# Kernel optimization log

Measured on AMD Instinct MI355X. Metric: run time of the kernel, lower is better.

The kernel has to match this reference:

```python
import jax, jax.numpy as jnp
import numpy as np

N_NODES = 200000
N_EDGES = 240000
HIDDEN = 128
N_TYPES = 6


def setup_inputs() -> dict:
    key = jax.random.key(0)
    k1, k2, k3, k4, k5 = jax.random.split(key, 5)
    state_embedding = jax.random.normal(k1, (N_NODES, HIDDEN), dtype=jnp.float32)
    # row 0: edge type in [1, N_TYPES]; row 1: source node; row 2: target node
    etype = jax.random.randint(k2, (N_EDGES,), 1, N_TYPES + 1, dtype=jnp.int32)
    src = jax.random.randint(k3, (N_EDGES,), 0, N_NODES, dtype=jnp.int32)
    tgt = jax.random.randint(k4, (N_EDGES,), 0, N_NODES, dtype=jnp.int32)
    typed_edges = jnp.stack([etype, src, tgt], axis=0)  # [3, E]
    # stacked per-edge-type Linear(2H, H, bias=False) weights, applied as x @ W[t]
    W = jax.random.normal(k5, (N_TYPES, 2 * HIDDEN, HIDDEN), dtype=jnp.float32) / np.sqrt(2 * HIDDEN)
    return {"state_embedding": state_embedding, "typed_edges": typed_edges, "W": W}


def reference(state_embedding, typed_edges, W):
    etype, src, tgt = typed_edges[0], typed_edges[1], typed_edges[2]
    # gather source/target node states and concat -> [E, 2H]
    x = jnp.concatenate([state_embedding[src], state_embedding[tgt]], axis=1)
    n_types = W.shape[0]
    msgs = jnp.zeros((x.shape[0], W.shape[2]), dtype=x.dtype)
    # fixed small loop over edge types; masking replaces the dynamic boolean
    # filtering of the torch code (edges with type t use only W[t-1])
    for t in range(n_types):
        mask = (etype == t + 1)[:, None]
        msgs = msgs + jnp.where(mask, x @ W[t], jnp.zeros((), x.dtype))
    # scatter-add messages into target node slots, dim_size = num nodes
    return jax.ops.segment_sum(msgs, tgt, num_segments=state_embedding.shape[0])
```

## Files before the change

### kernel.cpp

```cpp
#include <hip/hip_runtime.h>

#define NTYPES 6
#define HID 128
#define E_TILE 64
#define TPB 4
#define TNBITS 19
#define TNMASK ((1 << TNBITS) - 1)

typedef short short8 __attribute__((ext_vector_type(8)));
typedef float f32x4 __attribute__((ext_vector_type(4)));

static __device__ __forceinline__ ushort f2bf(float f) {
    union { float f; unsigned u; } v; v.f = f;
    unsigned r = v.u + 0x7FFFu + ((v.u >> 16) & 1u);
    return (ushort)(r >> 16);
}


__global__ void k_prep(int4* __restrict__ zp, int n4,
                       const float* __restrict__ Sf, ushort* __restrict__ Sb, int total,
                       const float* __restrict__ W, ushort* __restrict__ Wt,
                       int zb, int sb) {
    int b = blockIdx.x;
    if (b < zb) {
        int i = b * 256 + threadIdx.x;
        if (i < n4) zp[i] = make_int4(0, 0, 0, 0);
    } else if (b < zb + sb) {
        int g = ((b - zb) * 256 + threadIdx.x) * 8;
        if (g < total) {
            float4 a = *(const float4*)(Sf + g);
            float4 c = *(const float4*)(Sf + g + 4);
            ushort t[8] = { f2bf(a.x), f2bf(a.y), f2bf(a.z), f2bf(a.w),
                            f2bf(c.x), f2bf(c.y), f2bf(c.z), f2bf(c.w) };
            *(short8*)(Sb + g) = *(short8*)t;
        }
    } else {
        int t = (b - zb - sb) * 256 + threadIdx.x;
        int n  = t & 127;
        int k8 = (t >> 7) & 31;
        int ty = t >> 12;
        if (ty >= NTYPES) return;
        const float* wp = W + ((size_t)ty * 256 + (size_t)k8 * 8) * HID + n;
        ushort tmp[8];
        #pragma unroll
        for (int j = 0; j < 8; ++j) tmp[j] = f2bf(wp[(size_t)j * HID]);
        *(short8*)(Wt + ((size_t)ty * HID + n) * 256 + k8 * 8) = *(short8*)tmp;
    }
}

template <int RANK>
__global__ void k_bin(const int* __restrict__ etype, const int* __restrict__ src,
                      const int* __restrict__ tgt, int E, int CAP,
                      int* __restrict__ hdr, int* __restrict__ ncnt,
                      int2* __restrict__ sortedT2) {
    __shared__ int lcnt[NTYPES];
    __shared__ int lbase[NTYPES];
    if (threadIdx.x < NTYPES) lcnt[threadIdx.x] = 0;
    __syncthreads();
    int i = blockIdx.x * 256 + threadIdx.x;
    bool valid = (i < E);
    int sn = 0, pk = 0, t = 0, lrk = 0;
    if (valid) {
        t  = etype[i] - 1;
        int tn = tgt[i];
        sn = src[i];
        int a = 0;
        if (RANK) a = atomicAdd(&ncnt[tn], 1);
        pk  = tn | (a << TNBITS);
        lrk = atomicAdd(&lcnt[t], 1);
    }
    __syncthreads();
    if (threadIdx.x < NTYPES) {
        int c = lcnt[threadIdx.x];
        lbase[threadIdx.x] = c ? atomicAdd(&hdr[16 + threadIdx.x], c) : 0;
    }
    __syncthreads();
    if (valid) {
        int pos = lbase[t] + lrk;
        if (pos < CAP) sortedT2[(size_t)t * CAP + pos] = make_int2(sn, pk);
    }
}

__global__ void k_scan1(const int* __restrict__ ncnt, int* __restrict__ noff,
                        int* __restrict__ bsum, int N) {
    __shared__ int s[256];
    const int b = blockIdx.x, t = threadIdx.x;
    const int base = b * 1024 + t * 4;
    int v[4];
    #pragma unroll
    for (int i = 0; i < 4; ++i) v[i] = (base + i < N) ? ncnt[base + i] : 0;
    int tsum = v[0] + v[1] + v[2] + v[3];
    s[t] = tsum;
    __syncthreads();
    for (int off = 1; off < 256; off <<= 1) {
        int x = (t >= off) ? s[t - off] : 0;
        __syncthreads();
        s[t] += x;
        __syncthreads();
    }
    if (t == 255) bsum[b] = s[255];
    int run = s[t] - tsum;
    #pragma unroll
    for (int i = 0; i < 4; ++i)
        if (base + i < N) { noff[base + i] = run; run += v[i]; }
}

__global__ void k_scan2(int* __restrict__ bsum, int nb) {
    __shared__ int s[256];
    const int t = threadIdx.x;
    int v = (t < nb) ? bsum[t] : 0;
    s[t] = v;
    __syncthreads();
    for (int off = 1; off < 256; off <<= 1) {
        int x = (t >= off) ? s[t - off] : 0;
        __syncthreads();
        s[t] += x;
        __syncthreads();
    }
    if (t < nb) bsum[t] = s[t] - v;
}

template <int MODE>
__launch_bounds__(256, 4)
__global__ void k_gemm(const ushort* __restrict__ Sb, const float* __restrict__ Sf,
                       const ushort* __restrict__ Wt, const int* __restrict__ hdr,
                       const int2* __restrict__ sortedT2, int CAP,
                       const int* __restrict__ ncnt, const int* __restrict__ noff,
                       const int* __restrict__ bsum,
                       ushort* __restrict__ msgs, float* __restrict__ out) {
    __shared__ __align__(16) ushort Xs[E_TILE][264];
    __shared__ int sN[TPB][E_TILE];
    __shared__ int tN[TPB][E_TILE];
    __shared__ int dstR[TPB][E_TILE];

    int g = blockIdx.x;
    int ty, t0 = 0, ntl = 0, cnt_t = 0;
    for (ty = 0; ty < NTYPES; ++ty) {
        int c = hdr[16 + ty];
        if (c > CAP) c = CAP;
        int nt = (c + E_TILE - 1) >> 6;
        int ng = (nt + TPB - 1) / TPB;
        if (g < ng) {
            t0 = g * TPB;
            ntl = nt - t0; if (ntl > TPB) ntl = TPB;
            cnt_t = c;
            break;
        }
        g -= ng;
    }
    if (ty == NTYPES) return;

    const int tid = threadIdx.x;
    const int w  = tid >> 6;
    const int l  = tid & 63;
    const int lr = l & 15;
    const int lg = l >> 4;

    {
        const int tt = tid >> 6, s = l;
        if (tt < ntl) {
            int gp = (t0 + tt) * E_TILE + s;
            int sn = 0, tn = 0, dr = 0;
            if (gp < cnt_t) {
                int2 v = sortedT2[(size_t)ty * CAP + gp];
                sn = v.x;
                tn = v.y & TNMASK;
                if (MODE == 2) {
                    int a = ((unsigned)v.y) >> TNBITS;
                    dr = (ncnt[tn] == 1) ? -(tn + 1)
                                         : (noff[tn] + bsum[tn >> 10] + a);
                }
            }
            sN[tt][s] = sn; tN[tt][s] = tn; dstR[tt][s] = dr;
        }
    }
    __syncthreads();

    const ushort* wb = Wt + ((size_t)ty * HID + w * 32 + lr) * 256 + 8 * lg;

    for (int tt = 0; tt < ntl; ++tt) {
        int cnt = cnt_t - (t0 + tt) * E_TILE;
        if (cnt > E_TILE) cnt = E_TILE;

        {
            const int e = tid >> 2, q = tid & 3;
            ushort* dp = &Xs[e][q * 64];
            if (e < cnt) {
                const int node = (q & 2) ? tN[tt][e] : sN[tt][e];
                if (MODE == 2) {
                    const ushort* rp = Sb + (size_t)node * HID + (q & 1) * 64;
                    short8 v[8];
                    #pragma unroll
                    for (int i = 0; i < 8; ++i) v[i] = *(const short8*)(rp + i * 8);
                    #pragma unroll
                    for (int i = 0; i < 8; ++i) *(short8*)(dp + i * 8) = v[i];
                } else {
                    const float* rp = Sf + (size_t)node * HID + (q & 1) * 64;
                    #pragma unroll
                    for (int i = 0; i < 8; ++i) {
                        float4 a = *(const float4*)(rp + i * 8);
                        float4 b = *(const float4*)(rp + i * 8 + 4);
                        ushort tmp[8] = { f2bf(a.x), f2bf(a.y), f2bf(a.z), f2bf(a.w),
                                          f2bf(b.x), f2bf(b.y), f2bf(b.z), f2bf(b.w) };
                        *(short8*)(dp + i * 8) = *(short8*)tmp;
                    }
                }
            } else {
                short8 z = (short8){0, 0, 0, 0, 0, 0, 0, 0};
                #pragma unroll
                for (int i = 0; i < 8; ++i) *(short8*)(dp + i * 8) = z;
            }
        }
        __syncthreads();

        f32x4 acc[4][2];
        #pragma unroll
        for (int mf = 0; mf < 4; ++mf)
            #pragma unroll
            for (int nf = 0; nf < 2; ++nf)
                acc[mf][nf] = (f32x4){0.f, 0.f, 0.f, 0.f};

        const ushort* xb = &Xs[lr][8 * lg];
        #pragma unroll
        for (int kk = 0; kk < 8; ++kk) {
            const int k0 = kk * 32;
            short8 b0 = *(const short8*)(wb + k0);
            short8 b1 = *(const short8*)(wb + 16 * 256 + k0);
            #pragma unroll
            for (int mf = 0; mf < 4; ++mf) {
                short8 a = *(const short8*)(xb + mf * 16 * 264 + k0);
                acc[mf][0] = __builtin_amdgcn_mfma_f32_16x16x32_bf16(a, b0, acc[mf][0], 0, 0, 0);
                acc[mf][1] = __builtin_amdgcn_mfma_f32_16x16x32_bf16(a, b1, acc[mf][1], 0, 0, 0);
            }
        }
        __syncthreads();

        float (*Os)[132] = (float (*)[132])&Xs[0][0];
        #pragma unroll
        for (int mf = 0; mf < 4; ++mf)
            #pragma unroll
            for (int nf = 0; nf < 2; ++nf)
                #pragma unroll
                for (int r = 0; r < 4; ++r)
                    Os[mf * 16 + lg * 4 + r][w * 32 + nf * 16 + lr] = acc[mf][nf][r];
        __syncthreads();

        if (MODE == 2) {
            const int r8e = tid >> 4, cg = tid & 15;
            #pragma unroll
            for (int rr = 0; rr < 4; ++rr) {
                int row = rr * 16 + r8e;
                if (row < cnt) {
                    int dr = dstR[tt][row];
                    float4 a = *(const float4*)&Os[row][cg * 8];
                    float4 b = *(const float4*)&Os[row][cg * 8 + 4];
                    if (dr >= 0) {
                        ushort tmp[8] = { f2bf(a.x), f2bf(a.y), f2bf(a.z), f2bf(a.w),
                                          f2bf(b.x), f2bf(b.y), f2bf(b.z), f2bf(b.w) };
                        *(short8*)(msgs + (size_t)dr * HID + cg * 8) = *(short8*)tmp;
                    } else {
                        float* op = out + (size_t)(-dr - 1) * HID + cg * 8;
                        *(float4*)op = a;
                        *(float4*)(op + 4) = b;
                    }
                }
            }
        } else {
            const int rA = tid >> 7;
            const int c  = tid & (HID - 1);
            for (int it = 0; it < E_TILE / 2; ++it) {
                int ee = it * 2 + rA;
                if (ee < cnt) atomicAdd(&out[(size_t)tN[tt][ee] * HID + c], Os[ee][c]);
            }
        }
        __syncthreads();
    }
}

__launch_bounds__(256)
__global__ void k_scatter(const ushort* __restrict__ msgs, const int* __restrict__ noff,
                          const int* __restrict__ bsum, float* __restrict__ out,
                          int N, int Etot) {
    int node = blockIdx.x * 4 + (threadIdx.x >> 6);
    if (node >= N) return;
    int cp = threadIdx.x & 63;
    int s = noff[node] + bsum[node >> 10];
    int e = (node + 1 < N) ? (noff[node + 1] + bsum[(node + 1) >> 10]) : Etot;
    if (e - s == 1) return;
    float a0 = 0.f, a1 = 0.f;
    for (int r = s; r < e; ++r) {
        unsigned u = *(const unsigned*)(msgs + (size_t)r * HID + cp * 2);
        union { unsigned u; float f; } lo, hi;
        lo.u = u << 16; hi.u = u & 0xFFFF0000u;
        a0 += lo.f; a1 += hi.f;
    }
    *(float2*)(out + (size_t)node * HID + cp * 2) = make_float2(a0, a1);
}

extern "C" void kernel_launch(void* const* d_in, const int* in_sizes, int n_in,
                              void* d_out, int out_size, void* d_ws, size_t ws_size,
                              hipStream_t stream) {
    const float* Sf    = (const float*)d_in[0];
    const int*   edges = (const int*)d_in[1];
    const float* W     = (const float*)d_in[2];
    float* out = (float*)d_out;

    const int E = in_sizes[1] / 3;
    const int N = in_sizes[0] / HID;
    const int* etype = edges;
    const int* src   = edges + E;
    const int* tgt   = edges + 2 * E;
    int* ws = (int*)d_ws;

    const int CAP = E / 5 + 4096;

    int* ncnt = ws + 32;
    int* noff = ncnt + N;
    int* bsum = noff + N + 1;
    size_t intsEnd = (size_t)(32 + N + (N + 1) + 256) * sizeof(int);
    size_t st2Off  = (intsEnd + 255) & ~(size_t)255;
    size_t wtOff   = ((st2Off + (size_t)NTYPES * CAP * sizeof(int2)) + 255) & ~(size_t)255;
    size_t sbOff   = ((wtOff + (size_t)NTYPES * HID * 256 * 2) + 255) & ~(size_t)255;
    size_t msgsOff = ((sbOff + (size_t)N * HID * 2) + 255) & ~(size_t)255;
    size_t need2   = msgsOff + (size_t)E * HID * 2;

    const int nb1 = (N + 1023) / 1024;
    const int eb  = (E + 255) / 256;
    const int nblocks = (E + E_TILE * TPB - 1) / (E_TILE * TPB) + 2 * NTYPES;
    ushort* Wt = (ushort*)((char*)d_ws + wtOff);
    int2* sortedT2 = (int2*)((char*)d_ws + st2Off);

    if (ws_size >= need2 && nb1 <= 256 && N < (1 << TNBITS)) {
        ushort* Sb   = (ushort*)((char*)d_ws + sbOff);
        ushort* msgs = (ushort*)((char*)d_ws + msgsOff);
        const int total = N * HID;
        const int n4 = (32 + N + 3) / 4;
        const int zb = (n4 + 255) / 256;
        const int sb = (total / 8 + 255) / 256;
        const int wb = (NTYPES * HID * 32 + 255) / 256;

        k_prep<<<zb + sb + wb, 256, 0, stream>>>((int4*)ws, n4, Sf, Sb, total, W, Wt, zb, sb);
        k_bin<1><<<eb, 256, 0, stream>>>(etype, src, tgt, E, CAP, ws, ncnt, sortedT2);
        k_scan1<<<nb1, 256, 0, stream>>>(ncnt, noff, bsum, N);
        k_scan2<<<1, 256, 0, stream>>>(bsum, nb1);
        k_gemm<2><<<nblocks, 256, 0, stream>>>(Sb, Sf, Wt, ws, sortedT2, CAP,
                                               ncnt, noff, bsum, msgs, out);
        k_scatter<<<(N + 3) / 4, 256, 0, stream>>>(msgs, noff, bsum, out, N, E);
    } else {
        int2* sortedT0 = (int2*)((char*)d_ws + 256);
        ushort* Wt0 = (ushort*)((char*)d_ws + 256 +
                      (((size_t)NTYPES * CAP * sizeof(int2) + 255) & ~(size_t)255));

        k_prep<<<1 + (NTYPES * HID * 32 + 255) / 256, 256, 0, stream>>>(
            (int4*)ws, 8, nullptr, nullptr, 0, W, Wt0, 1, 0);
        hipMemsetAsync(d_out, 0, (size_t)out_size * sizeof(float), stream);
        k_bin<0><<<eb, 256, 0, stream>>>(etype, src, tgt, E, CAP, ws, nullptr, sortedT0);
        k_gemm<0><<<nblocks, 256, 0, stream>>>(nullptr, Sf, Wt0, ws, sortedT0, CAP,
                                               nullptr, nullptr, nullptr, nullptr, out);
    }
}
```

Baseline: 132.0 us.

## Prefetch next edge tile into registers and pack degree-1 flag into offsets

The bf16 gather of the next tile's source and target node rows is now issued into registers before the current tile's MFMA work, so global-load latency can overlap compute. A degree-1 flag is packed into the high bit of each node offset during the scan, so the gemm and scatter kernels skip reading the separate count array and the next node's offset for degree-1 nodes. The prefetch raises register pressure under a launch bound of four blocks per CU, and the packed flag limits offsets to 30 bits.

```diff
diff --git a/kernel.cpp b/kernel.cpp
--- a/kernel.cpp
+++ b/kernel.cpp
@@ -6,6 +6,8 @@
 #define TPB 4
 #define TNBITS 19
 #define TNMASK ((1 << TNBITS) - 1)
+#define DEG1F 0x40000000
+#define OFFM  0x3FFFFFFF
 
 typedef short short8 __attribute__((ext_vector_type(8)));
 typedef float f32x4 __attribute__((ext_vector_type(4)));
@@ -102,7 +104,10 @@
     int run = s[t] - tsum;
     #pragma unroll
     for (int i = 0; i < 4; ++i)
-        if (base + i < N) { noff[base + i] = run; run += v[i]; }
+        if (base + i < N) {
+            noff[base + i] = run | ((v[i] == 1) ? DEG1F : 0);
+            run += v[i];
+        }
 }
 
 __global__ void k_scan2(int* __restrict__ bsum, int nb) {
@@ -125,8 +130,7 @@
 __global__ void k_gemm(const ushort* __restrict__ Sb, const float* __restrict__ Sf,
                        const ushort* __restrict__ Wt, const int* __restrict__ hdr,
                        const int2* __restrict__ sortedT2, int CAP,
-                       const int* __restrict__ ncnt, const int* __restrict__ noff,
-                       const int* __restrict__ bsum,
+                       const int* __restrict__ noff, const int* __restrict__ bsum,
                        ushort* __restrict__ msgs, float* __restrict__ out) {
     __shared__ __align__(16) ushort Xs[E_TILE][264];
     __shared__ int sN[TPB][E_TILE];
@@ -167,8 +171,9 @@
                 tn = v.y & TNMASK;
                 if (MODE == 2) {
                     int a = ((unsigned)v.y) >> TNBITS;
-                    dr = (ncnt[tn] == 1) ? -(tn + 1)
-                                         : (noff[tn] + bsum[tn >> 10] + a);
+                    int nf_ = noff[tn];
+                    dr = (nf_ & DEG1F) ? -(tn + 1)
+                                       : ((nf_ & OFFM) + bsum[tn >> 10] + a);
                 }
             }
             sN[tt][s] = sn; tN[tt][s] = tn; dstR[tt][s] = dr;
@@ -177,41 +182,64 @@
     __syncthreads();
 
     const ushort* wb = Wt + ((size_t)ty * HID + w * 32 + lr) * 256 + 8 * lg;
+
+    const int e_ = tid >> 2, q_ = tid & 3;
+    const short8 z8 = (short8){0, 0, 0, 0, 0, 0, 0, 0};
+    short8 pv[8];
+
+    if (MODE == 2) {
+        int cnt0 = cnt_t - t0 * E_TILE; if (cnt0 > E_TILE) cnt0 = E_TILE;
+        if (e_ < cnt0) {
+            const int node = (q_ & 2) ? tN[0][e_] : sN[0][e_];
+            const ushort* rp = Sb + (size_t)node * HID + (q_ & 1) * 64;
+            #pragma unroll
+            for (int i = 0; i < 8; ++i) pv[i] = *(const short8*)(rp + i * 8);
+        } else {
+            #pragma unroll
+            for (int i = 0; i < 8; ++i) pv[i] = z8;
+        }
+    }
 
     for (int tt = 0; tt < ntl; ++tt) {
         int cnt = cnt_t - (t0 + tt) * E_TILE;
         if (cnt > E_TILE) cnt = E_TILE;
 
-        {
-            const int e = tid >> 2, q = tid & 3;
-            ushort* dp = &Xs[e][q * 64];
-            if (e < cnt) {
-                const int node = (q & 2) ? tN[tt][e] : sN[tt][e];
-                if (MODE == 2) {
-                    const ushort* rp = Sb + (size_t)node * HID + (q & 1) * 64;
-                    short8 v[8];
-                    #pragma unroll
-                    for (int i = 0; i < 8; ++i) v[i] = *(const short8*)(rp + i * 8);
-                    #pragma unroll
-                    for (int i = 0; i < 8; ++i) *(short8*)(dp + i * 8) = v[i];
-                } else {
-                    const float* rp = Sf + (size_t)node * HID + (q & 1) * 64;
-                    #pragma unroll
-                    for (int i = 0; i < 8; ++i) {
-                        float4 a = *(const float4*)(rp + i * 8);
-                        float4 b = *(const float4*)(rp + i * 8 + 4);
-                        ushort tmp[8] = { f2bf(a.x), f2bf(a.y), f2bf(a.z), f2bf(a.w),
-                                          f2bf(b.x), f2bf(b.y), f2bf(b.z), f2bf(b.w) };
-                        *(short8*)(dp + i * 8) = *(short8*)tmp;
-                    }
+        if (MODE == 2) {
+            ushort* dp = &Xs[e_][q_ * 64];
+            #pragma unroll
+            for (int i = 0; i < 8; ++i) *(short8*)(dp + i * 8) = pv[i];
+        } else {
+            ushort* dp = &Xs[e_][q_ * 64];
+            if (e_ < cnt) {
+                const int node = (q_ & 2) ? tN[tt][e_] : sN[tt][e_];
+                const float* rp = Sf + (size_t)node * HID + (q_ & 1) * 64;
+                #pragma unroll
+                for (int i = 0; i < 8; ++i) {
+                    float4 a = *(const float4*)(rp + i * 8);
+                    float4 b = *(const float4*)(rp + i * 8 + 4);
+                    ushort tmp[8] = { f2bf(a.x), f2bf(a.y), f2bf(a.z), f2bf(a.w),
+                                      f2bf(b.x), f2bf(b.y), f2bf(b.z), f2bf(b.w) };
+                    *(short8*)(dp + i * 8) = *(short8*)tmp;
                 }
             } else {
-                short8 z = (short8){0, 0, 0, 0, 0, 0, 0, 0};
-                #pragma unroll
-                for (int i = 0; i < 8; ++i) *(short8*)(dp + i * 8) = z;
-            }
-        }
-        __syncthreads();
+                #pragma unroll
+                for (int i = 0; i < 8; ++i) *(short8*)(dp + i * 8) = z8;
+            }
+        }
+        __syncthreads();
+
+        if (MODE == 2 && tt + 1 < ntl) {
+            int cntn = cnt_t - (t0 + tt + 1) * E_TILE; if (cntn > E_TILE) cntn = E_TILE;
+            if (e_ < cntn) {
+                const int node = (q_ & 2) ? tN[tt + 1][e_] : sN[tt + 1][e_];
+                const ushort* rp = Sb + (size_t)node * HID + (q_ & 1) * 64;
+                #pragma unroll
+                for (int i = 0; i < 8; ++i) pv[i] = *(const short8*)(rp + i * 8);
+            } else {
+                #pragma unroll
+                for (int i = 0; i < 8; ++i) pv[i] = z8;
+            }
+        }
 
         f32x4 acc[4][2];
         #pragma unroll
@@ -283,10 +311,11 @@
                           int N, int Etot) {
     int node = blockIdx.x * 4 + (threadIdx.x >> 6);
     if (node >= N) return;
+    int raw = noff[node];
+    if (raw & DEG1F) return;
     int cp = threadIdx.x & 63;
-    int s = noff[node] + bsum[node >> 10];
-    int e = (node + 1 < N) ? (noff[node + 1] + bsum[(node + 1) >> 10]) : Etot;
-    if (e - s == 1) return;
+    int s = (raw & OFFM) + bsum[node >> 10];
+    int e = (node + 1 < N) ? ((noff[node + 1] & OFFM) + bsum[(node + 1) >> 10]) : Etot;
     float a0 = 0.f, a1 = 0.f;
     for (int r = s; r < e; ++r) {
         unsigned u = *(const unsigned*)(msgs + (size_t)r * HID + cp * 2);
@@ -344,7 +373,7 @@
         k_scan1<<<nb1, 256, 0, stream>>>(ncnt, noff, bsum, N);
         k_scan2<<<1, 256, 0, stream>>>(bsum, nb1);
         k_gemm<2><<<nblocks, 256, 0, stream>>>(Sb, Sf, Wt, ws, sortedT2, CAP,
-                                               ncnt, noff, bsum, msgs, out);
+                                               noff, bsum, msgs, out);
         k_scatter<<<(N + 3) / 4, 256, 0, stream>>>(msgs, noff, bsum, out, N, E);
     } else {
         int2* sortedT0 = (int2*)((char*)d_ws + 256);
@@ -356,6 +385,6 @@
         hipMemsetAsync(d_out, 0, (size_t)out_size * sizeof(float), stream);
         k_bin<0><<<eb, 256, 0, stream>>>(etype, src, tgt, E, CAP, ws, nullptr, sortedT0);
         k_gemm<0><<<nblocks, 256, 0, stream>>>(nullptr, Sf, Wt0, ws, sortedT0, CAP,
-                                               nullptr, nullptr, nullptr, nullptr, out);
-    }
-}
+                                               nullptr, nullptr, nullptr, out);
+    }
+}
```

Measured after the change: 157.3 us. +19.2%, slower.
